# Performance work log

Measured on AMD Instinct MI355X. Metric: run time of the kernel, lower is better.

## Reference

```python
import jax, jax.numpy as jnp
import numpy as np

HEADS = 16

def setup_inputs() -> dict:
    key = jax.random.key(0)
    ks = jax.random.split(key, 9)
    b, n, d, kp = 2, 4096, 1024, 2048
    s = lambda fan: 1.0 / np.sqrt(fan)
    x = jax.random.normal(ks[0], (b, n, d), jnp.float32)
    mask = jax.random.randint(ks[1], (n, n), 0, 2).astype(jnp.float32)  # 1 = masked out
    Wq = jax.random.normal(ks[2], (d, d), jnp.float32) * s(d)
    Wk = jax.random.normal(ks[3], (d, d), jnp.float32) * s(d)
    Wv = jax.random.normal(ks[4], (d, d), jnp.float32) * s(d)
    Wo = jax.random.normal(ks[5], (d, d), jnp.float32) * s(d)
    bo = jnp.zeros((d,), jnp.float32)
    proj_k = jax.random.normal(ks[6], (n, kp), jnp.float32) * s(n)
    proj_v = jax.random.normal(ks[7], (n, kp), jnp.float32) * s(n)
    return {"x": x, "mask": mask, "Wq": Wq, "Wk": Wk, "Wv": Wv,
            "Wo": Wo, "bo": bo, "proj_k": proj_k, "proj_v": proj_v}


def reference(x, mask, Wq, Wk, Wv, Wo, bo, proj_k, proj_v):
    b, n, d = x.shape
    h = HEADS
    dh = d // h
    kp = proj_k.shape[1]

    q = x @ Wq                                   # [b, n, d]
    k = jnp.einsum('bnd,nk->bkd', x @ Wk, proj_k)  # [b, kp, d] Linformer K compression
    v = jnp.einsum('bnd,nk->bkd', x @ Wv, proj_v)  # [b, kp, d]

    q = q.reshape(b, n, h, dh).transpose(0, 2, 1, 3)    # [b, h, n, dh]
    k = k.reshape(b, kp, h, dh).transpose(0, 2, 1, 3)   # [b, h, kp, dh]
    v = v.reshape(b, kp, h, dh).transpose(0, 2, 1, 3)   # [b, h, kp, dh]

    # tf.image.resize nearest (half-pixel centers): width n -> kp, height n -> n (identity)
    col_idx = jnp.floor((jnp.arange(kp) + 0.5) * (n / kp)).astype(jnp.int32)
    m = mask[:, col_idx][None, None]             # [1, 1, n, kp]

    scores = jnp.einsum('bhnd,bhkd->bhnk', q, k) / jnp.sqrt(jnp.float32(dh))
    scores = scores + m * (-1e9)
    attn = jax.nn.softmax(scores, axis=-1)       # dropout = identity at inference

    out = jnp.einsum('bhnk,bhkd->bhnd', attn, v)
    out = out.transpose(0, 2, 1, 3).reshape(b, n, d)
    return out @ Wo + bo
```

## Files before the change

### kernel.cpp

```cpp
#include <hip/hip_runtime.h>
#include <stdint.h>

using u16 = unsigned short;
typedef __bf16 bf16x8 __attribute__((ext_vector_type(8)));
typedef float f32x4 __attribute__((ext_vector_type(4)));
typedef u16 ushort8 __attribute__((ext_vector_type(8)));
typedef unsigned uint4v __attribute__((ext_vector_type(4)));
typedef unsigned uint2v __attribute__((ext_vector_type(2)));


__device__ __forceinline__ u16 f2bf(float f) {
    unsigned u = __builtin_bit_cast(unsigned, f);
    return (u16)((u + 0x7fffu + ((u >> 16) & 1u)) >> 16);
}

__device__ __forceinline__ float bf2f(u16 v) {
    unsigned u = (unsigned)v << 16;
    return __builtin_bit_cast(float, u);
}

__device__ __forceinline__ float fexp2(float x) {
#if __has_builtin(__builtin_amdgcn_exp2f)
    return __builtin_amdgcn_exp2f(x);
#else
    return exp2f(x);
#endif
}

__device__ __forceinline__ unsigned cvt_pk_bf16(float lo, float hi) {
    unsigned r;
    asm("v_cvt_pk_bf16_f32 %0, %1, %2" : "=v"(r) : "v"(lo), "v"(hi));
    return r;
}

#define GLD16(gptr, lptr) __builtin_amdgcn_global_load_lds( \
    (const __attribute__((address_space(1))) void*)(unsigned long long)(gptr), \
    (__attribute__((address_space(3))) void*)(unsigned)(unsigned long long)(lptr), 16, 0, 0)


__global__ void convert_bf16(const float* __restrict__ in, u16* __restrict__ out) {
    int gid = blockIdx.x * 256 + threadIdx.x;
    const float4* in4 = (const float4*)in;
    float4 a = in4[2 * gid], b = in4[2 * gid + 1];
    ushort8 o;
    o[0] = f2bf(a.x); o[1] = f2bf(a.y); o[2] = f2bf(a.z); o[3] = f2bf(a.w);
    o[4] = f2bf(b.x); o[5] = f2bf(b.y); o[6] = f2bf(b.z); o[7] = f2bf(b.w);
    *(ushort8*)(out + (size_t)gid * 8) = o;
}

__global__ void transpose_convert(const float* __restrict__ in, u16* __restrict__ out,
                                  int R, int C) {
    __shared__ u16 sT[64][65];
    const int c0 = blockIdx.x << 6, r0 = blockIdx.y << 6;
    const int tid = threadIdx.x;
#pragma unroll
    for (int rep = 0; rep < 16; rep++) {
        int idx = rep * 256 + tid;
        int r = idx >> 6, c = idx & 63;
        sT[c][r] = f2bf(in[(size_t)(r0 + r) * C + c0 + c]);
    }
    __syncthreads();
#pragma unroll
    for (int rep = 0; rep < 16; rep++) {
        int idx = rep * 256 + tid;
        int r = idx >> 6, c = idx & 63;
        out[(size_t)(c0 + r) * R + r0 + c] = sT[r][c];
    }
}

__global__ void mask_pack(const float* __restrict__ mask, unsigned* __restrict__ mw) {
    int gid = blockIdx.x * 256 + threadIdx.x;
    int i = gid >> 11, j = gid & 2047;
    float v = mask[(size_t)i * 4096 + 2 * j + 1];
    unsigned long long b = __ballot(v != 0.0f);
    int lane = threadIdx.x & 63;
    if (lane == 0)       mw[(size_t)i * 64 + (j >> 5)] = (unsigned)b;
    else if (lane == 32) mw[(size_t)i * 64 + (j >> 5)] = (unsigned)(b >> 32);
}


template <bool OUT_BF16, bool ADD_BIAS>
__global__ __launch_bounds__(256) void gemm_nt(
    const u16* __restrict__ A, int lda, long long sA,
    const u16* __restrict__ B, int ldb, long long sB,
    void* __restrict__ Cp, int ldc, long long sC,
    const float* __restrict__ bias, int K) {
    __shared__ __align__(16) u16 lds[2][2][4][128][8];
    const int bz = blockIdx.z;
    const u16* Ab = A + (size_t)sA * bz;
    const u16* Bb = B + (size_t)sB * bz;
    const int m0 = blockIdx.y << 7, n0 = blockIdx.x << 7;
    const int tid = threadIdx.x, wave = tid >> 6, lane = tid & 63;
    const int kg = lane >> 4, lr = lane & 15;
    const int wr = (wave >> 1) << 6, wc = (wave & 1) << 6;
    const int nT = K >> 5;
    f32x4 acc[4][4] = {};

#pragma unroll
    for (int i = 0; i < 2; i++) {
        int row = i * 64 + lane;
        GLD16(Ab + (size_t)(m0 + row) * lda + wave * 8, &lds[0][0][wave][i * 64][0]);
        GLD16(Bb + (size_t)(n0 + row) * ldb + wave * 8, &lds[0][1][wave][i * 64][0]);
    }
    for (int t = 0; t < nT; ++t) {
        const int cur = t & 1;
        if (t + 1 < nT) {
            const int nxt = cur ^ 1;
            const int koff = (t + 1) << 5;
#pragma unroll
            for (int i = 0; i < 2; i++) {
                int row = i * 64 + lane;
                GLD16(Ab + (size_t)(m0 + row) * lda + koff + wave * 8, &lds[nxt][0][wave][i * 64][0]);
                GLD16(Bb + (size_t)(n0 + row) * ldb + koff + wave * 8, &lds[nxt][1][wave][i * 64][0]);
            }
        }
        __syncthreads();
        bf16x8 af[4], bfv[4];
#pragma unroll
        for (int mi = 0; mi < 4; mi++)
            af[mi] = *(const bf16x8*)&lds[cur][0][kg][wr + mi * 16 + lr][0];
#pragma unroll
        for (int ni = 0; ni < 4; ni++)
            bfv[ni] = *(const bf16x8*)&lds[cur][1][kg][wc + ni * 16 + lr][0];
#pragma unroll
        for (int mi = 0; mi < 4; mi++)
#pragma unroll
            for (int ni = 0; ni < 4; ni++)
                acc[mi][ni] = __builtin_amdgcn_mfma_f32_16x16x32_bf16(af[mi], bfv[ni], acc[mi][ni], 0, 0, 0);
        __syncthreads();
    }

    if constexpr (OUT_BF16) {
        u16* C = (u16*)Cp + (size_t)sC * bz;
#pragma unroll
        for (int mi = 0; mi < 4; mi++)
#pragma unroll
            for (int ni = 0; ni < 4; ni++)
#pragma unroll
                for (int r = 0; r < 4; r++) {
                    int gr = m0 + wr + mi * 16 + kg * 4 + r;
                    int gc = n0 + wc + ni * 16 + lr;
                    C[(size_t)gr * ldc + gc] = f2bf(acc[mi][ni][r]);
                }
    } else {
        float* C = (float*)Cp + (size_t)sC * bz;
#pragma unroll
        for (int mi = 0; mi < 4; mi++)
#pragma unroll
            for (int ni = 0; ni < 4; ni++)
#pragma unroll
                for (int r = 0; r < 4; r++) {
                    int gr = m0 + wr + mi * 16 + kg * 4 + r;
                    int gc = n0 + wc + ni * 16 + lr;
                    float v = acc[mi][ni][r];
                    if constexpr (ADD_BIAS) v += bias[gc];
                    C[(size_t)gr * ldc + gc] = v;
                }
    }
}

__global__ __launch_bounds__(256) void gemm_nt_splitk(
    const u16* __restrict__ A, int lda, long long sAb,
    const u16* __restrict__ B, int ldb, long long sBb,
    u16* __restrict__ Cp, int ldc, long long sC, int K2) {
    __shared__ __align__(16) u16 lds[2][2][4][128][8];
    const int bz = blockIdx.z, bsel = bz >> 1, ks = bz & 1;
    const u16* Ab = A + (size_t)sAb * bsel + (size_t)ks * K2;
    const u16* Bb = B + (size_t)sBb * bsel + (size_t)ks * K2;
    const int m0 = blockIdx.y << 7, n0 = blockIdx.x << 7;
    const int tid = threadIdx.x, wave = tid >> 6, lane = tid & 63;
    const int kg = lane >> 4, lr = lane & 15;
    const int wr = (wave >> 1) << 6, wc = (wave & 1) << 6;
    const int nT = K2 >> 5;
    f32x4 acc[4][4] = {};

#pragma unroll
    for (int i = 0; i < 2; i++) {
        int row = i * 64 + lane;
        GLD16(Ab + (size_t)(m0 + row) * lda + wave * 8, &lds[0][0][wave][i * 64][0]);
        GLD16(Bb + (size_t)(n0 + row) * ldb + wave * 8, &lds[0][1][wave][i * 64][0]);
    }
    for (int t = 0; t < nT; ++t) {
        const int cur = t & 1;
        if (t + 1 < nT) {
            const int nxt = cur ^ 1;
            const int koff = (t + 1) << 5;
#pragma unroll
            for (int i = 0; i < 2; i++) {
                int row = i * 64 + lane;
                GLD16(Ab + (size_t)(m0 + row) * lda + koff + wave * 8, &lds[nxt][0][wave][i * 64][0]);
                GLD16(Bb + (size_t)(n0 + row) * ldb + koff + wave * 8, &lds[nxt][1][wave][i * 64][0]);
            }
        }
        __syncthreads();
        bf16x8 af[4], bfv[4];
#pragma unroll
        for (int mi = 0; mi < 4; mi++)
            af[mi] = *(const bf16x8*)&lds[cur][0][kg][wr + mi * 16 + lr][0];
#pragma unroll
        for (int ni = 0; ni < 4; ni++)
            bfv[ni] = *(const bf16x8*)&lds[cur][1][kg][wc + ni * 16 + lr][0];
#pragma unroll
        for (int mi = 0; mi < 4; mi++)
#pragma unroll
            for (int ni = 0; ni < 4; ni++)
                acc[mi][ni] = __builtin_amdgcn_mfma_f32_16x16x32_bf16(af[mi], bfv[ni], acc[mi][ni], 0, 0, 0);
        __syncthreads();
    }

    u16* C = Cp + (size_t)sC * bz;
#pragma unroll
    for (int mi = 0; mi < 4; mi++)
#pragma unroll
        for (int ni = 0; ni < 4; ni++)
#pragma unroll
            for (int r = 0; r < 4; r++) {
                int gr = m0 + wr + mi * 16 + kg * 4 + r;
                int gc = n0 + wc + ni * 16 + lr;
                C[(size_t)gr * ldc + gc] = f2bf(acc[mi][ni][r]);
            }
}

__global__ void combine_bf16(const u16* __restrict__ p, u16* __restrict__ dst) {
    int gid = blockIdx.x * 256 + threadIdx.x;
    size_t d = (size_t)gid * 8;
    size_t b = d >> 21, r = d & (((size_t)1 << 21) - 1);
    const ushort8 a = *(const ushort8*)(p + ((b * 2) << 21) + r);
    const ushort8 c = *(const ushort8*)(p + ((b * 2 + 1) << 21) + r);
    ushort8 o;
#pragma unroll
    for (int i = 0; i < 8; i++) o[i] = f2bf(bf2f(a[i]) + bf2f(c[i]));
    *(ushort8*)(dst + d) = o;
}


__global__ __launch_bounds__(256) void attn_kernel(
    const u16* __restrict__ q, const u16* __restrict__ kb,
    const u16* __restrict__ vt, const unsigned* __restrict__ mw,
    u16* __restrict__ ao) {
    __shared__ __align__(16) u16 sK[2][8][32][8];
    __shared__ __align__(16) u16 sV[2][4][64][8];
    const int tid = threadIdx.x;
    const int wave = tid >> 6, lane = tid & 63, kg = lane >> 4, lr = lane & 15;
    const int b = blockIdx.x >> 4, h = blockIdx.x & 15;
    const int nrow = (blockIdx.y << 6) + wave * 16;

    const u16* qrow = q + (size_t)(b * 4096 + nrow + lr) * 1024 + h * 64 + kg * 8;
    const bf16x8 aq0 = *(const bf16x8*)qrow;
    const bf16x8 aq1 = *(const bf16x8*)(qrow + 32);
    const u16* kh = kb + (size_t)b * 2048 * 1024 + h * 64;
    const u16* vh = vt + ((size_t)b * 1024 + (size_t)h * 64) * 2048;
    const unsigned* mrow = mw + (size_t)(nrow + lr) * 64;

    const u16* ksrc = kh + (size_t)(lane & 31) * 1024 + (wave * 2 + (lane >> 5)) * 8;
    const u16* vsrc = vh + (size_t)lane * 2048 + wave * 8;

    f32x4 o[4] = {};
    float lsum = 0.0f;
    const bool low16 = (lane & 16) == 0;

    auto stage = [&](int bf, int j0) {
        GLD16(ksrc + (size_t)j0 * 1024, &sK[bf][wave * 2][0][0]);
        GLD16(vsrc + j0, &sV[bf][wave][0][0]);
    };

    auto process = [&](int cur, unsigned wd) {
        const bf16x8 k0a = *(const bf16x8*)&sK[cur][kg][lr][0];
        const bf16x8 k0b = *(const bf16x8*)&sK[cur][4 + kg][lr][0];
        const bf16x8 k1a = *(const bf16x8*)&sK[cur][kg][16 + lr][0];
        const bf16x8 k1b = *(const bf16x8*)&sK[cur][4 + kg][16 + lr][0];
        const bf16x8 v0 = *(const bf16x8*)&sV[cur][kg][lr][0];
        const bf16x8 v1 = *(const bf16x8*)&sV[cur][kg][16 + lr][0];
        const bf16x8 v2 = *(const bf16x8*)&sV[cur][kg][32 + lr][0];
        const bf16x8 v3 = *(const bf16x8*)&sV[cur][kg][48 + lr][0];

        f32x4 s0 = {0.f, 0.f, 0.f, 0.f}, s1 = {0.f, 0.f, 0.f, 0.f};
        s0 = __builtin_amdgcn_mfma_f32_16x16x32_bf16(k0a, aq0, s0, 0, 0, 0);
        s0 = __builtin_amdgcn_mfma_f32_16x16x32_bf16(k0b, aq1, s0, 0, 0, 0);
        s1 = __builtin_amdgcn_mfma_f32_16x16x32_bf16(k1a, aq0, s1, 0, 0, 0);
        s1 = __builtin_amdgcn_mfma_f32_16x16x32_bf16(k1b, aq1, s1, 0, 0, 0);
        const unsigned mb0 = wd >> (kg * 4);
        const unsigned mb1 = wd >> (16 + kg * 4);
        const float C = 0.18033688f;
        float p0[4], p1[4];
#pragma unroll
        for (int r = 0; r < 4; r++) {
            float t0 = ((mb0 >> r) & 1u) ? -1.0e30f : s0[r] * C;
            float t1 = ((mb1 >> r) & 1u) ? -1.0e30f : s1[r] * C;
            p0[r] = fexp2(t0);
            p1[r] = fexp2(t1);
            lsum += p0[r] + p1[r];
        }
        unsigned X0 = cvt_pk_bf16(p0[0], p0[1]);
        unsigned X1 = cvt_pk_bf16(p0[2], p0[3]);
        unsigned Y0 = cvt_pk_bf16(p1[0], p1[1]);
        unsigned Y1 = cvt_pk_bf16(p1[2], p1[3]);
        asm volatile("v_permlane32_swap_b32 %0, %1" : "+v"(X0), "+v"(Y0));
        asm volatile("v_permlane32_swap_b32 %0, %1" : "+v"(X1), "+v"(Y1));
        unsigned sX0 = (unsigned)__shfl_xor((int)X0, 16);
        unsigned sY0 = (unsigned)__shfl_xor((int)Y0, 16);
        unsigned sX1 = (unsigned)__shfl_xor((int)X1, 16);
        unsigned sY1 = (unsigned)__shfl_xor((int)Y1, 16);
        uint4v wv;
        wv[0] = low16 ? X0 : sY0;
        wv[1] = low16 ? X1 : sY1;
        wv[2] = low16 ? sX0 : Y0;
        wv[3] = low16 ? sX1 : Y1;
        bf16x8 W = __builtin_bit_cast(bf16x8, wv);
        o[0] = __builtin_amdgcn_mfma_f32_16x16x32_bf16(v0, W, o[0], 0, 0, 0);
        o[1] = __builtin_amdgcn_mfma_f32_16x16x32_bf16(v1, W, o[1], 0, 0, 0);
        o[2] = __builtin_amdgcn_mfma_f32_16x16x32_bf16(v2, W, o[2], 0, 0, 0);
        o[3] = __builtin_amdgcn_mfma_f32_16x16x32_bf16(v3, W, o[3], 0, 0, 0);
    };

    stage(0, 0);
    for (int t = 0; t < 64; ++t) {
        const int cur = t & 1;
        if (t < 63) stage(cur ^ 1, (t + 1) * 32);
        __syncthreads();
        process(cur, mrow[t]);
        __syncthreads();
    }

    lsum += __shfl_xor(lsum, 16);
    lsum += __shfl_xor(lsum, 32);
    const float inv = 1.0f / lsum;

    u16* orow = ao + (size_t)(b * 4096 + nrow + lr) * 1024 + h * 64 + kg * 4;
#pragma unroll
    for (int f = 0; f < 4; f++) {
        uint2v st;
        st[0] = cvt_pk_bf16(o[f][0] * inv, o[f][1] * inv);
        st[1] = cvt_pk_bf16(o[f][2] * inv, o[f][3] * inv);
        *(uint2v*)(orow + f * 16) = st;
    }
}


extern "C" void kernel_launch(void* const* d_in, const int* in_sizes, int n_in,
                              void* d_out, int out_size, void* d_ws, size_t ws_size,
                              hipStream_t stream) {
    const float* x    = (const float*)d_in[0];
    const float* mask = (const float*)d_in[1];
    const float* Wq   = (const float*)d_in[2];
    const float* Wk   = (const float*)d_in[3];
    const float* Wv   = (const float*)d_in[4];
    const float* Wo   = (const float*)d_in[5];
    const float* bo   = (const float*)d_in[6];
    const float* pk   = (const float*)d_in[7];
    const float* pv   = (const float*)d_in[8];
    float* out = (float*)d_out;

    char* w = (char*)d_ws;
    auto alloc = [&](size_t bytes) { void* p = w; w += (bytes + 255) & ~(size_t)255; return p; };
    u16* xb   = (u16*)alloc((size_t)8192 * 1024 * 2);
    u16* qb   = (u16*)alloc((size_t)8192 * 1024 * 2);
    u16* xkT  = (u16*)alloc((size_t)1024 * 8192 * 2);
    u16* xvT  = (u16*)alloc((size_t)1024 * 8192 * 2);
    u16* WqT  = (u16*)alloc((size_t)1024 * 1024 * 2);
    u16* WkT  = (u16*)alloc((size_t)1024 * 1024 * 2);
    u16* WvT  = (u16*)alloc((size_t)1024 * 1024 * 2);
    u16* WoT  = (u16*)alloc((size_t)1024 * 1024 * 2);
    u16* pkT  = (u16*)alloc((size_t)2048 * 4096 * 2);
    u16* pvT  = (u16*)alloc((size_t)2048 * 4096 * 2);
    u16* kbuf = (u16*)alloc((size_t)2 * 2048 * 1024 * 2);
    u16* vtb  = (u16*)alloc((size_t)2 * 1024 * 2048 * 2);
    unsigned* mw = (unsigned*)alloc((size_t)4096 * 64 * 4);
    (void)alloc((size_t)128 * 1024);
    u16* ao   = xb;
    u16* pbuf = qb;
    (void)xvT;

    convert_bf16<<<4096, 256, 0, stream>>>(x, xb);
    transpose_convert<<<dim3(16, 16), 256, 0, stream>>>(Wq, WqT, 1024, 1024);
    transpose_convert<<<dim3(16, 16), 256, 0, stream>>>(Wk, WkT, 1024, 1024);
    transpose_convert<<<dim3(16, 16), 256, 0, stream>>>(Wv, WvT, 1024, 1024);
    transpose_convert<<<dim3(16, 16), 256, 0, stream>>>(Wo, WoT, 1024, 1024);
    transpose_convert<<<dim3(32, 64), 256, 0, stream>>>(pk, pkT, 4096, 2048);
    transpose_convert<<<dim3(32, 64), 256, 0, stream>>>(pv, pvT, 4096, 2048);
    mask_pack<<<32768, 256, 0, stream>>>(mask, mw);

    gemm_nt<true, false><<<dim3(64, 16, 1), 256, 0, stream>>>(WkT, 1024, 0, xb, 1024, 0, xkT, 8192, 0, nullptr, 1024);

    gemm_nt_splitk<<<dim3(8, 16, 4), 256, 0, stream>>>(pkT, 4096, 0, xkT, 8192, 4096,
                                                       pbuf, 1024, (long long)1 << 21, 2048);
    combine_bf16<<<2048, 256, 0, stream>>>(pbuf, kbuf);
    gemm_nt_splitk<<<dim3(16, 8, 4), 256, 0, stream>>>(xvT, 8192, 4096, pvT, 4096, 0,
                                                       pbuf, 2048, (long long)1 << 21, 2048);
    combine_bf16<<<2048, 256, 0, stream>>>(pbuf, vtb);

    gemm_nt<true, false><<<dim3(8, 64, 1), 256, 0, stream>>>(xb, 1024, 0, WqT, 1024, 0, qb, 1024, 0, nullptr, 1024);

    attn_kernel<<<dim3(32, 64), 256, 0, stream>>>(qb, kbuf, vtb, mw, ao);

    gemm_nt<false, true><<<dim3(8, 64, 1), 256, 0, stream>>>(ao, 1024, 0, WoT, 1024, 0, out, 1024, 0, bo, 1024);
}
```

Measured before the change: 567.3 us.

## Process two 16-row query tiles per wave in attention kernel to reuse K/V loads

```diff
diff --git a/kernel.cpp b/kernel.cpp
--- a/kernel.cpp
+++ b/kernel.cpp
@@ -243,20 +243,24 @@
     const int tid = threadIdx.x;
     const int wave = tid >> 6, lane = tid & 63, kg = lane >> 4, lr = lane & 15;
     const int b = blockIdx.x >> 4, h = blockIdx.x & 15;
-    const int nrow = (blockIdx.y << 6) + wave * 16;
+    const int nrow = (blockIdx.y << 7) + wave * 32;
 
     const u16* qrow = q + (size_t)(b * 4096 + nrow + lr) * 1024 + h * 64 + kg * 8;
-    const bf16x8 aq0 = *(const bf16x8*)qrow;
-    const bf16x8 aq1 = *(const bf16x8*)(qrow + 32);
+    const bf16x8 aq00 = *(const bf16x8*)qrow;
+    const bf16x8 aq01 = *(const bf16x8*)(qrow + 32);
+    const bf16x8 aq10 = *(const bf16x8*)(qrow + 16 * 1024);
+    const bf16x8 aq11 = *(const bf16x8*)(qrow + 16 * 1024 + 32);
     const u16* kh = kb + (size_t)b * 2048 * 1024 + h * 64;
     const u16* vh = vt + ((size_t)b * 1024 + (size_t)h * 64) * 2048;
-    const unsigned* mrow = mw + (size_t)(nrow + lr) * 64;
+    const unsigned* mrow0 = mw + (size_t)(nrow + lr) * 64;
+    const unsigned* mrow1 = mrow0 + 16 * 64;
 
     const u16* ksrc = kh + (size_t)(lane & 31) * 1024 + (wave * 2 + (lane >> 5)) * 8;
     const u16* vsrc = vh + (size_t)lane * 2048 + wave * 8;
 
-    f32x4 o[4] = {};
-    float lsum = 0.0f;
+    f32x4 o0[4] = {};
+    f32x4 o1[4] = {};
+    float lsum0 = 0.0f, lsum1 = 0.0f;
     const bool low16 = (lane & 16) == 0;
 
     auto stage = [&](int bf, int j0) {
@@ -264,33 +268,7 @@
         GLD16(vsrc + j0, &sV[bf][wave][0][0]);
     };
 
-    auto process = [&](int cur, unsigned wd) {
-        const bf16x8 k0a = *(const bf16x8*)&sK[cur][kg][lr][0];
-        const bf16x8 k0b = *(const bf16x8*)&sK[cur][4 + kg][lr][0];
-        const bf16x8 k1a = *(const bf16x8*)&sK[cur][kg][16 + lr][0];
-        const bf16x8 k1b = *(const bf16x8*)&sK[cur][4 + kg][16 + lr][0];
-        const bf16x8 v0 = *(const bf16x8*)&sV[cur][kg][lr][0];
-        const bf16x8 v1 = *(const bf16x8*)&sV[cur][kg][16 + lr][0];
-        const bf16x8 v2 = *(const bf16x8*)&sV[cur][kg][32 + lr][0];
-        const bf16x8 v3 = *(const bf16x8*)&sV[cur][kg][48 + lr][0];
-
-        f32x4 s0 = {0.f, 0.f, 0.f, 0.f}, s1 = {0.f, 0.f, 0.f, 0.f};
-        s0 = __builtin_amdgcn_mfma_f32_16x16x32_bf16(k0a, aq0, s0, 0, 0, 0);
-        s0 = __builtin_amdgcn_mfma_f32_16x16x32_bf16(k0b, aq1, s0, 0, 0, 0);
-        s1 = __builtin_amdgcn_mfma_f32_16x16x32_bf16(k1a, aq0, s1, 0, 0, 0);
-        s1 = __builtin_amdgcn_mfma_f32_16x16x32_bf16(k1b, aq1, s1, 0, 0, 0);
-        const unsigned mb0 = wd >> (kg * 4);
-        const unsigned mb1 = wd >> (16 + kg * 4);
-        const float C = 0.18033688f;
-        float p0[4], p1[4];
-#pragma unroll
-        for (int r = 0; r < 4; r++) {
-            float t0 = ((mb0 >> r) & 1u) ? -1.0e30f : s0[r] * C;
-            float t1 = ((mb1 >> r) & 1u) ? -1.0e30f : s1[r] * C;
-            p0[r] = fexp2(t0);
-            p1[r] = fexp2(t1);
-            lsum += p0[r] + p1[r];
-        }
+    auto xform = [&](const float p0[4], const float p1[4]) -> bf16x8 {
         unsigned X0 = cvt_pk_bf16(p0[0], p0[1]);
         unsigned X1 = cvt_pk_bf16(p0[2], p0[3]);
         unsigned Y0 = cvt_pk_bf16(p1[0], p1[1]);
@@ -306,33 +284,83 @@
         wv[1] = low16 ? X1 : sY1;
         wv[2] = low16 ? sX0 : Y0;
         wv[3] = low16 ? sX1 : Y1;
-        bf16x8 W = __builtin_bit_cast(bf16x8, wv);
-        o[0] = __builtin_amdgcn_mfma_f32_16x16x32_bf16(v0, W, o[0], 0, 0, 0);
-        o[1] = __builtin_amdgcn_mfma_f32_16x16x32_bf16(v1, W, o[1], 0, 0, 0);
-        o[2] = __builtin_amdgcn_mfma_f32_16x16x32_bf16(v2, W, o[2], 0, 0, 0);
-        o[3] = __builtin_amdgcn_mfma_f32_16x16x32_bf16(v3, W, o[3], 0, 0, 0);
+        return __builtin_bit_cast(bf16x8, wv);
     };
 
+    auto process = [&](int cur, unsigned wd0, unsigned wd1) {
+        const bf16x8 k0a = *(const bf16x8*)&sK[cur][kg][lr][0];
+        const bf16x8 k0b = *(const bf16x8*)&sK[cur][4 + kg][lr][0];
+        const bf16x8 k1a = *(const bf16x8*)&sK[cur][kg][16 + lr][0];
+        const bf16x8 k1b = *(const bf16x8*)&sK[cur][4 + kg][16 + lr][0];
+        const bf16x8 v0 = *(const bf16x8*)&sV[cur][kg][lr][0];
+        const bf16x8 v1 = *(const bf16x8*)&sV[cur][kg][16 + lr][0];
+        const bf16x8 v2 = *(const bf16x8*)&sV[cur][kg][32 + lr][0];
+        const bf16x8 v3 = *(const bf16x8*)&sV[cur][kg][48 + lr][0];
+
+        f32x4 s00 = {}, s01 = {}, s10 = {}, s11 = {};
+        s00 = __builtin_amdgcn_mfma_f32_16x16x32_bf16(k0a, aq00, s00, 0, 0, 0);
+        s00 = __builtin_amdgcn_mfma_f32_16x16x32_bf16(k0b, aq01, s00, 0, 0, 0);
+        s01 = __builtin_amdgcn_mfma_f32_16x16x32_bf16(k1a, aq00, s01, 0, 0, 0);
+        s01 = __builtin_amdgcn_mfma_f32_16x16x32_bf16(k1b, aq01, s01, 0, 0, 0);
+        s10 = __builtin_amdgcn_mfma_f32_16x16x32_bf16(k0a, aq10, s10, 0, 0, 0);
+        s10 = __builtin_amdgcn_mfma_f32_16x16x32_bf16(k0b, aq11, s10, 0, 0, 0);
+        s11 = __builtin_amdgcn_mfma_f32_16x16x32_bf16(k1a, aq10, s11, 0, 0, 0);
+        s11 = __builtin_amdgcn_mfma_f32_16x16x32_bf16(k1b, aq11, s11, 0, 0, 0);
+
+        const float C = 0.18033688f;
+        const unsigned mb00 = wd0 >> (kg * 4), mb01 = wd0 >> (16 + kg * 4);
+        const unsigned mb10 = wd1 >> (kg * 4), mb11 = wd1 >> (16 + kg * 4);
+        float p00[4], p01[4], p10[4], p11[4];
+#pragma unroll
+        for (int r = 0; r < 4; r++) {
+            p00[r] = fexp2(((mb00 >> r) & 1u) ? -1.0e30f : s00[r] * C);
+            p01[r] = fexp2(((mb01 >> r) & 1u) ? -1.0e30f : s01[r] * C);
+            p10[r] = fexp2(((mb10 >> r) & 1u) ? -1.0e30f : s10[r] * C);
+            p11[r] = fexp2(((mb11 >> r) & 1u) ? -1.0e30f : s11[r] * C);
+            lsum0 += p00[r] + p01[r];
+            lsum1 += p10[r] + p11[r];
+        }
+        const bf16x8 W0 = xform(p00, p01);
+        const bf16x8 W1 = xform(p10, p11);
+        o0[0] = __builtin_amdgcn_mfma_f32_16x16x32_bf16(v0, W0, o0[0], 0, 0, 0);
+        o0[1] = __builtin_amdgcn_mfma_f32_16x16x32_bf16(v1, W0, o0[1], 0, 0, 0);
+        o0[2] = __builtin_amdgcn_mfma_f32_16x16x32_bf16(v2, W0, o0[2], 0, 0, 0);
+        o0[3] = __builtin_amdgcn_mfma_f32_16x16x32_bf16(v3, W0, o0[3], 0, 0, 0);
+        o1[0] = __builtin_amdgcn_mfma_f32_16x16x32_bf16(v0, W1, o1[0], 0, 0, 0);
+        o1[1] = __builtin_amdgcn_mfma_f32_16x16x32_bf16(v1, W1, o1[1], 0, 0, 0);
+        o1[2] = __builtin_amdgcn_mfma_f32_16x16x32_bf16(v2, W1, o1[2], 0, 0, 0);
+        o1[3] = __builtin_amdgcn_mfma_f32_16x16x32_bf16(v3, W1, o1[3], 0, 0, 0);
+    };
+
     stage(0, 0);
+    unsigned wdc0 = mrow0[0], wdc1 = mrow1[0];
     for (int t = 0; t < 64; ++t) {
         const int cur = t & 1;
         if (t < 63) stage(cur ^ 1, (t + 1) * 32);
-        __syncthreads();
-        process(cur, mrow[t]);
-        __syncthreads();
-    }
-
-    lsum += __shfl_xor(lsum, 16);
-    lsum += __shfl_xor(lsum, 32);
-    const float inv = 1.0f / lsum;
-
-    u16* orow = ao + (size_t)(b * 4096 + nrow + lr) * 1024 + h * 64 + kg * 4;
+        unsigned wdn0 = (t < 63) ? mrow0[t + 1] : 0u;
+        unsigned wdn1 = (t < 63) ? mrow1[t + 1] : 0u;
+        __syncthreads();
+        process(cur, wdc0, wdc1);
+        wdc0 = wdn0;
+        wdc1 = wdn1;
+        __syncthreads();
+    }
+
+    lsum0 += __shfl_xor(lsum0, 16); lsum0 += __shfl_xor(lsum0, 32);
+    lsum1 += __shfl_xor(lsum1, 16); lsum1 += __shfl_xor(lsum1, 32);
+    const float inv0 = 1.0f / lsum0, inv1 = 1.0f / lsum1;
+
+    u16* orow0 = ao + (size_t)(b * 4096 + nrow + lr) * 1024 + h * 64 + kg * 4;
+    u16* orow1 = orow0 + 16 * 1024;
 #pragma unroll
     for (int f = 0; f < 4; f++) {
-        uint2v st;
-        st[0] = cvt_pk_bf16(o[f][0] * inv, o[f][1] * inv);
-        st[1] = cvt_pk_bf16(o[f][2] * inv, o[f][3] * inv);
-        *(uint2v*)(orow + f * 16) = st;
+        uint2v st0, st1;
+        st0[0] = cvt_pk_bf16(o0[f][0] * inv0, o0[f][1] * inv0);
+        st0[1] = cvt_pk_bf16(o0[f][2] * inv0, o0[f][3] * inv0);
+        st1[0] = cvt_pk_bf16(o1[f][0] * inv1, o1[f][1] * inv1);
+        st1[1] = cvt_pk_bf16(o1[f][2] * inv1, o1[f][3] * inv1);
+        *(uint2v*)(orow0 + f * 16) = st0;
+        *(uint2v*)(orow1 + f * 16) = st1;
     }
 }
 
@@ -391,7 +419,7 @@
 
     gemm_nt<true, false><<<dim3(8, 64, 1), 256, 0, stream>>>(xb, 1024, 0, WqT, 1024, 0, qb, 1024, 0, nullptr, 1024);
 
-    attn_kernel<<<dim3(32, 64), 256, 0, stream>>>(qb, kbuf, vtb, mw, ao);
+    attn_kernel<<<dim3(32, 32), 256, 0, stream>>>(qb, kbuf, vtb, mw, ao);
 
     gemm_nt<false, true><<<dim3(8, 64, 1), 256, 0, stream>>>(ao, 1024, 0, WoT, 1024, 0, out, 1024, 0, bo, 1024);
 }
```

Result: no change. 571.0 us (+0.7%).
